# Kernel optimization log

Hardware: AMD Instinct MI355X
Metric: run time of the kernel (lower is better)

The kernel has to match this reference:

```python
import jax, jax.numpy as jnp
import numpy as np

NUM_USERS = 100_000
NUM_JOBS = 100_000
N_NODES = NUM_USERS + NUM_JOBS
E = 3_200_000
D = 64  # embedding_dim == hidden_dim
B = 16_384


def setup_inputs() -> dict:
    key = jax.random.key(0)
    ks = jax.random.split(key, 10)
    edge_index = jax.random.randint(ks[0], (2, E), 0, N_NODES, dtype=jnp.int64)
    user_indices = jax.random.randint(ks[1], (B,), 0, NUM_USERS, dtype=jnp.int64)
    job_indices = jax.random.randint(ks[2], (B,), 0, NUM_JOBS, dtype=jnp.int64)
    # parameters (match reset_parameters: embeddings std=0.1, xavier pred, zero bias)
    user_emb_w = 0.1 * jax.random.normal(ks[3], (NUM_USERS, D), dtype=jnp.float32)
    job_emb_w = 0.1 * jax.random.normal(ks[4], (NUM_JOBS, D), dtype=jnp.float32)
    W1 = jax.random.normal(ks[5], (D, D), dtype=jnp.float32) / np.sqrt(D)
    b1 = jnp.zeros((D,), dtype=jnp.float32)
    W2 = jax.random.normal(ks[6], (D, D), dtype=jnp.float32) / np.sqrt(D)
    b2 = jnp.zeros((D,), dtype=jnp.float32)
    lim = np.sqrt(6.0 / (2 * D + 1))
    pred_w = jax.random.uniform(ks[7], (2 * D, 1), dtype=jnp.float32, minval=-lim, maxval=lim)
    pred_b = jnp.zeros((1,), dtype=jnp.float32)
    return {
        "edge_index": edge_index, "user_indices": user_indices, "job_indices": job_indices,
        "user_emb_w": user_emb_w, "job_emb_w": job_emb_w,
        "W1": W1, "b1": b1, "W2": W2, "b2": b2,
        "pred_w": pred_w, "pred_b": pred_b,
    }


def reference(edge_index, user_indices, job_indices, user_emb_w, job_emb_w, W1, b1, W2, b2, pred_w, pred_b):
    num_users = user_emb_w.shape[0]
    n = num_users + job_emb_w.shape[0]
    x = jnp.concatenate([user_emb_w, job_emb_w], axis=0)  # [N, D]

    # GCNConv (PyG defaults): add self-loops, symmetric D^-1/2 (A+I) D^-1/2 normalization
    loops = jnp.arange(n, dtype=edge_index.dtype)
    row = jnp.concatenate([edge_index[0], loops])  # source nodes
    col = jnp.concatenate([edge_index[1], loops])  # target nodes
    deg = jax.ops.segment_sum(jnp.ones_like(col, dtype=x.dtype), col, num_segments=n)
    dinv = jnp.where(deg > 0, jax.lax.rsqrt(jnp.maximum(deg, 1e-12)), 0.0)
    norm = dinv[row] * dinv[col]  # [E+N]

    def gcn_conv(h, W, b):
        h = h @ W                                   # [N, D]
        msg = h[row] * norm[:, None]                # gather + scale, [E+N, D]
        agg = jax.ops.segment_sum(msg, col, num_segments=n)  # scatter-add
        return agg + b

    x = jax.nn.relu(gcn_conv(x, W1, b1))  # dropout is identity at inference
    x = gcn_conv(x, W2, b2)

    user_emb = x[user_indices]                      # [B, D]
    job_emb = x[num_users + job_indices]            # [B, D]
    combined = jnp.concatenate([user_emb, job_emb], axis=1)  # [B, 2D]
    return (combined @ pred_w + pred_b)[:, 0]       # [B]
```

## Files before the change

### kernel.cpp

```cpp
#include <hip/hip_runtime.h>
#include <hip/hip_fp16.h>

#define D 64
#define BSHIFT 10
#define BMASK ((1 << BSHIFT) - 1)
#define NBUK_MAX 256
#define T_TILE 6144
#define CAP 20480

#if defined(__has_builtin)
#if __has_builtin(__builtin_amdgcn_fdot2)
#define HAVE_FDOT2 1
#endif
#endif

typedef _Float16 h2f __attribute__((ext_vector_type(2)));
typedef _Float16 half8v __attribute__((ext_vector_type(8)));
typedef float f4v __attribute__((ext_vector_type(4)));

__device__ __forceinline__ int wave_iscan(int v, int lane) {
#pragma unroll
    for (int off = 1; off < 64; off <<= 1) {
        int u = __shfl_up(v, off, 64);
        if (lane >= off) v += u;
    }
    return v;
}

__device__ __forceinline__ int block_escan(int v, int tid, int* wtot ) {
    int lane = tid & 63, w = tid >> 6;
    int inc = wave_iscan(v, lane);
    if (lane == 63) wtot[w] = inc;
    __syncthreads();
    int addv = 0;
#pragma unroll
    for (int q = 0; q < 4; q++) addv += (q < w) ? wtot[q] : 0;
    return inc - v + addv;
}

__device__ __forceinline__ float4 h4_to_f4(uint2 u) {
    __half2 a = *(__half2*)&u.x, b = *(__half2*)&u.y;
    float2 fa = __half22float2(a), fb = __half22float2(b);
    return make_float4(fa.x, fa.y, fb.x, fb.y);
}

__device__ __forceinline__ void acc_u2(float* acc, uint2 u) {
#ifdef HAVE_FDOT2
    h2f a0, a1;
    __builtin_memcpy(&a0, &u.x, 4);
    __builtin_memcpy(&a1, &u.y, 4);
    const h2f LO = {(_Float16)1.0f, (_Float16)0.0f};
    const h2f HI = {(_Float16)0.0f, (_Float16)1.0f};
    acc[0] = __builtin_amdgcn_fdot2(a0, LO, acc[0], false);
    acc[1] = __builtin_amdgcn_fdot2(a0, HI, acc[1], false);
    acc[2] = __builtin_amdgcn_fdot2(a1, LO, acc[2], false);
    acc[3] = __builtin_amdgcn_fdot2(a1, HI, acc[3], false);
#else
    float4 v = h4_to_f4(u);
    acc[0] += v.x; acc[1] += v.y; acc[2] += v.z; acc[3] += v.w;
#endif
}

__device__ __forceinline__ void acc_u4(float* acc, uint4 u) {
    uint2 a; a.x = u.x; a.y = u.y;
    uint2 b; b.x = u.z; b.y = u.w;
    acc_u2(acc, a);
    acc_u2(acc + 4, b);
}


__global__ __launch_bounds__(256) void k_bin(const int* __restrict__ row, const int* __restrict__ col,
                                             int E, int* __restrict__ bbase,
                                             unsigned* __restrict__ ebuf, int nbuk,
                                             const float* __restrict__ W1, const float* __restrict__ W2,
                                             __half* __restrict__ WT1, __half* __restrict__ WT2) {
    __shared__ int hist4[4][NBUK_MAX];
    __shared__ int sexcl[NBUK_MAX];
    __shared__ int cur4[4][NBUK_MAX];
    __shared__ int gbase[NBUK_MAX];
    __shared__ int wtot[4];
    __shared__ unsigned stage[T_TILE];
    __shared__ unsigned char sbuk[T_TILE];
    int tid = threadIdx.x;
    int w = tid >> 6;
    int tile0 = blockIdx.x * T_TILE;
    int cnt = min(T_TILE, E - tile0);

    if (blockIdx.x < 2) {
        const float* Ws = blockIdx.x ? W2 : W1;
        __half* Wd = blockIdx.x ? WT2 : WT1;
#pragma unroll
        for (int i = 0; i < 16; i++) {
            int f = i * 256 + tid;
            int k = f >> 6, c = f & 63;
            Wd[c * 64 + k] = __float2half(Ws[f]);
        }
    }

#pragma unroll
    for (int q = 0; q < 4; q++) hist4[q][tid] = 0;
    __syncthreads();
    for (int i = tid; i < cnt; i += 256)
        atomicAdd(&hist4[w][col[tile0 + i] >> BSHIFT], 1);
    __syncthreads();

    int h0 = hist4[0][tid], h1 = hist4[1][tid], h2 = hist4[2][tid], h3 = hist4[3][tid];
    int v = h0 + h1 + h2 + h3;
    int excl = block_escan(v, tid, wtot);
    sexcl[tid] = excl;
    cur4[0][tid] = excl;
    cur4[1][tid] = excl + h0;
    cur4[2][tid] = excl + h0 + h1;
    cur4[3][tid] = excl + h0 + h1 + h2;
    gbase[tid] = (v > 0 && tid < nbuk) ? (tid * CAP + atomicAdd(&bbase[tid], v)) : 0;
    __syncthreads();

    for (int i = tid; i < cnt; i += 256) {
        int r = row[tile0 + i];
        int c = col[tile0 + i];
        int b = c >> BSHIFT;
        int p = atomicAdd(&cur4[w][b], 1);
        stage[p] = ((unsigned)(c & BMASK) << 18) | (unsigned)r;
        sbuk[p] = (unsigned char)b;
    }
    __syncthreads();

    for (int i = tid; i < cnt; i += 256) {
        int b = sbuk[i];
        int gpos = gbase[b] + (i - sexcl[b]);
        ebuf[gpos] = stage[i];
    }
}


__global__ __launch_bounds__(256) void k_csr2a(const unsigned* __restrict__ ebuf,
                                               const int* __restrict__ bbase, int N,
                                               int2* __restrict__ rps, float* __restrict__ dinv,
                                               __half* __restrict__ h, __half* __restrict__ hs2) {
    __shared__ int lcnt[1 << BSHIFT];
    __shared__ int wtot[4];
    int tid = threadIdx.x;
    int c0 = blockIdx.x << BSHIFT;
    int nn = min(1 << BSHIFT, N - c0);
    int e0 = blockIdx.x * CAP, e1 = e0 + bbase[blockIdx.x];

    if (blockIdx.x == 0 && tid < 32) {
        uint2 z; z.x = 0u; z.y = 0u;
        if (tid < 16) *(uint2*)(h + (size_t)N * D + tid * 4) = z;
        else *(uint2*)(hs2 + (size_t)N * D + (tid - 16) * 4) = z;
    }

    for (int i = tid; i < (1 << BSHIFT); i += 256) lcnt[i] = 0;
    __syncthreads();
    for (int j = e0 + tid; j < e1; j += 256)
        atomicAdd(&lcnt[ebuf[j] >> 18], 1);
    __syncthreads();

    int c[4]; int s = 0;
#pragma unroll
    for (int i = 0; i < 4; i++) { c[i] = lcnt[tid * 4 + i]; s += c[i]; }
    int run = block_escan(s, tid, wtot);
#pragma unroll
    for (int i = 0; i < 4; i++) {
        int idx = tid * 4 + i;
        if (idx < nn) {
            int st = e0 + run;
            rps[c0 + idx] = make_int2(st, st + c[i]);
            dinv[c0 + idx] = rsqrtf((float)(c[i] + 1));
        }
        run += c[i];
    }
}


__device__ __forceinline__ void stage_Wt(const __half* __restrict__ WTg, __half* __restrict__ Wt, int tid) {
#pragma unroll
    for (int i = 0; i < 2; i++) {
        int f = (i * 256 + tid) * 8;
        int c = f >> 6, k = f & 63;
        *(half8v*)(Wt + c * 72 + k) = *(const half8v*)(WTg + f);
    }
}

__device__ __forceinline__ void gemm_compute(const __half* __restrict__ Xh, const __half* __restrict__ Wt,
                                             int n0, int N, const float* __restrict__ dinv,
                                             __half* __restrict__ out, int tid) {
    int lane = tid & 63;
    int wv = tid >> 6;
    int n16 = lane & 15, quad = lane >> 4;
    const __half* Xw = Xh + (wv * 16) * 72;
    half8v a0 = *(const half8v*)(Xw + n16 * 72 + quad * 8);
    half8v a1 = *(const half8v*)(Xw + n16 * 72 + quad * 8 + 32);
    f4v acc[4];
#pragma unroll
    for (int ct = 0; ct < 4; ct++) {
        acc[ct] = (f4v){0.f, 0.f, 0.f, 0.f};
        const __half* wp = Wt + (ct * 16 + n16) * 72;
        half8v b0 = *(const half8v*)(wp + quad * 8);
        half8v b1 = *(const half8v*)(wp + quad * 8 + 32);
        acc[ct] = __builtin_amdgcn_mfma_f32_16x16x32_f16(a0, b0, acc[ct], 0, 0, 0);
        acc[ct] = __builtin_amdgcn_mfma_f32_16x16x32_f16(a1, b1, acc[ct], 0, 0, 0);
    }
#pragma unroll
    for (int r = 0; r < 4; r++) {
        int node = n0 + wv * 16 + quad * 4 + r;
        if (node < N) {
            float dv = dinv[node];
#pragma unroll
            for (int ct = 0; ct < 4; ct++)
                out[(size_t)node * D + ct * 16 + n16] = __float2half(acc[ct][r] * dv);
        }
    }
}


__global__ __launch_bounds__(256) void k_csr2b_gemm1(const unsigned* __restrict__ ebuf,
                                                     const int2* __restrict__ rps,
                                                     const int* __restrict__ bbase,
                                                     int N, int nbuk, int* __restrict__ srcs,
                                                     const float* __restrict__ xu, const float* __restrict__ xj,
                                                     int U, const __half* __restrict__ WT1,
                                                     const float* __restrict__ dinv, __half* __restrict__ h) {
    __shared__ __align__(16) __half Xh[64 * 72];
    __shared__ __align__(16) __half Wt[64 * 72];
    int tid = threadIdx.x;
    if ((int)blockIdx.x < nbuk) {
        int* lcur = (int*)Xh;
        int c0 = blockIdx.x << BSHIFT;
        int e0 = blockIdx.x * CAP, e1 = e0 + bbase[blockIdx.x];
        for (int i = tid; i < (1 << BSHIFT); i += 256)
            lcur[i] = (c0 + i < N) ? rps[c0 + i].x : 0;
        __syncthreads();
        for (int j = e0 + tid; j < e1; j += 256) {
            unsigned pk = ebuf[j];
            int p = atomicAdd(&lcur[pk >> 18], 1);
            srcs[p] = (int)(pk & 0x3ffffu);
        }
    } else {
        int n0 = ((int)blockIdx.x - nbuk) * 64;
        stage_Wt(WT1, Wt, tid);
#pragma unroll
        for (int i = 0; i < 4; i++) {
            int e4 = i * 256 + tid;
            int nl = e4 >> 4, k4 = e4 & 15;
            int nn = n0 + nl;
            uint2 st; st.x = 0u; st.y = 0u;
            if (nn < N) {
                const float* src = (nn < U) ? (xu + (size_t)nn * D) : (xj + (size_t)(nn - U) * D);
                float4 v = *(const float4*)(src + k4 * 4);
                __half2 p0 = __floats2half2_rn(v.x, v.y);
                __half2 p1 = __floats2half2_rn(v.z, v.w);
                st.x = *(unsigned*)&p0; st.y = *(unsigned*)&p1;
            }
            *(uint2*)(Xh + nl * 72 + k4 * 4) = st;
        }
        __syncthreads();
        gemm_compute(Xh, Wt, n0, N, dinv, h, tid);
    }
}


__device__ __forceinline__ void gather8(float* acc, const __half* __restrict__ hs,
                                        const int2* __restrict__ rps,
                                        const int* __restrict__ srcs,
                                        int node, int N, int g, int t) {
    const __half* hp = hs + t * 8;
    int2 r = rps[node];
    int e0 = r.x, deg = r.y - r.x;
    for (int cb = 0; cb < deg; cb += 8) {
        int sv = (cb + t < deg) ? srcs[e0 + cb + t] : N;
        int base = g * 8;
        int s0 = __shfl(sv, base + 0, 64);
        int s1 = __shfl(sv, base + 1, 64);
        int s2 = __shfl(sv, base + 2, 64);
        int s3 = __shfl(sv, base + 3, 64);
        int s4 = __shfl(sv, base + 4, 64);
        int s5 = __shfl(sv, base + 5, 64);
        int s6 = __shfl(sv, base + 6, 64);
        int s7 = __shfl(sv, base + 7, 64);
        uint4 u0 = *(const uint4*)(hp + (size_t)s0 * D);
        uint4 u1 = *(const uint4*)(hp + (size_t)s1 * D);
        uint4 u2 = *(const uint4*)(hp + (size_t)s2 * D);
        uint4 u3 = *(const uint4*)(hp + (size_t)s3 * D);
        uint4 u4 = *(const uint4*)(hp + (size_t)s4 * D);
        uint4 u5 = *(const uint4*)(hp + (size_t)s5 * D);
        uint4 u6 = *(const uint4*)(hp + (size_t)s6 * D);
        uint4 u7 = *(const uint4*)(hp + (size_t)s7 * D);
        acc_u4(acc, u0);
        acc_u4(acc, u1);
        acc_u4(acc, u2);
        acc_u4(acc, u3);
        acc_u4(acc, u4);
        acc_u4(acc, u5);
        acc_u4(acc, u6);
        acc_u4(acc, u7);
    }
}


__global__ __launch_bounds__(256) void k_agg_gemm2(const __half* __restrict__ hs, const float* __restrict__ dinv,
                                                   const int2* __restrict__ rps, const int* __restrict__ srcs,
                                                   const float* __restrict__ bias, const __half* __restrict__ WT2,
                                                   int N, __half* __restrict__ hs2) {
    __shared__ __align__(16) __half Xh[64 * 72];
    __shared__ __align__(16) __half Wt[64 * 72];
    int tid = threadIdx.x;
    int lane = tid & 63;
    int w = tid >> 6;
    int g = lane >> 3, t = lane & 7;
    int n0 = blockIdx.x * 64;

    stage_Wt(WT2, Wt, tid);

    float4 ba = *(const float4*)(bias + t * 8);
    float4 bb = *(const float4*)(bias + t * 8 + 4);
#pragma unroll
    for (int rr = 0; rr < 2; rr++) {
        int nl = w * 16 + rr * 8 + g;
        int node = n0 + nl;
        uint4 st; st.x = 0u; st.y = 0u; st.z = 0u; st.w = 0u;
        if (node < N) {
            float acc[8] = {0.f, 0.f, 0.f, 0.f, 0.f, 0.f, 0.f, 0.f};
            gather8(acc, hs, rps, srcs, node, N, g, t);
            uint4 su = *(const uint4*)(hs + (size_t)node * D + t * 8);
            float4 sa = h4_to_f4(make_uint2(su.x, su.y));
            float4 sb = h4_to_f4(make_uint2(su.z, su.w));
            float dv = dinv[node];
            float o0 = fmaxf((acc[0] + sa.x) * dv + ba.x, 0.f);
            float o1 = fmaxf((acc[1] + sa.y) * dv + ba.y, 0.f);
            float o2 = fmaxf((acc[2] + sa.z) * dv + ba.z, 0.f);
            float o3 = fmaxf((acc[3] + sa.w) * dv + ba.w, 0.f);
            float o4 = fmaxf((acc[4] + sb.x) * dv + bb.x, 0.f);
            float o5 = fmaxf((acc[5] + sb.y) * dv + bb.y, 0.f);
            float o6 = fmaxf((acc[6] + sb.z) * dv + bb.z, 0.f);
            float o7 = fmaxf((acc[7] + sb.w) * dv + bb.w, 0.f);
            __half2 p0 = __floats2half2_rn(o0, o1);
            __half2 p1 = __floats2half2_rn(o2, o3);
            __half2 p2 = __floats2half2_rn(o4, o5);
            __half2 p3 = __floats2half2_rn(o6, o7);
            st.x = *(unsigned*)&p0; st.y = *(unsigned*)&p1;
            st.z = *(unsigned*)&p2; st.w = *(unsigned*)&p3;
        }
        *(uint4*)(Xh + nl * 72 + t * 8) = st;
    }
    __syncthreads();
    gemm_compute(Xh, Wt, n0, N, dinv, hs2, tid);
}


__global__ __launch_bounds__(256) void k_pred(const __half* __restrict__ hs2, const float* __restrict__ dinv,
                                              const int2* __restrict__ rps, const int* __restrict__ srcs,
                                              const float* __restrict__ b2, const float* __restrict__ pw,
                                              const float* __restrict__ pb,
                                              const int* __restrict__ uidx, const int* __restrict__ jidx,
                                              int U, int N, int B, float* __restrict__ out) {
    int tid = threadIdx.x;
    int lane = tid & 63;
    int g = lane >> 3, t = lane & 7;
    int pair = blockIdx.x * 16 + (tid >> 6) * 4 + (g >> 1);
    if (pair >= B) return;
    int side = g & 1;
    int c = side ? (U + jidx[pair]) : uidx[pair];
    float acc[8] = {0.f, 0.f, 0.f, 0.f, 0.f, 0.f, 0.f, 0.f};
    gather8(acc, hs2, rps, srcs, c, N, g, t);
    uint4 su = *(const uint4*)(hs2 + (size_t)c * D + t * 8);
    float4 sa = h4_to_f4(make_uint2(su.x, su.y));
    float4 sb = h4_to_f4(make_uint2(su.z, su.w));
    float4 bva = *(const float4*)(b2 + t * 8);
    float4 bvb = *(const float4*)(b2 + t * 8 + 4);
    float dv = dinv[c];
    float4 wa = *(const float4*)(pw + side * 64 + t * 8);
    float4 wb = *(const float4*)(pw + side * 64 + t * 8 + 4);
    float vx = ((acc[0] + sa.x) * dv + bva.x) * wa.x
             + ((acc[1] + sa.y) * dv + bva.y) * wa.y
             + ((acc[2] + sa.z) * dv + bva.z) * wa.z
             + ((acc[3] + sa.w) * dv + bva.w) * wa.w
             + ((acc[4] + sb.x) * dv + bvb.x) * wb.x
             + ((acc[5] + sb.y) * dv + bvb.y) * wb.y
             + ((acc[6] + sb.z) * dv + bvb.z) * wb.z
             + ((acc[7] + sb.w) * dv + bvb.w) * wb.w;
    vx += __shfl_xor(vx, 1, 64); vx += __shfl_xor(vx, 2, 64);
    vx += __shfl_xor(vx, 4, 64);
    vx += __shfl_xor(vx, 8, 64);
    if ((lane & 15) == 0) out[pair] = vx + pb[0];
}


extern "C" void kernel_launch(void* const* d_in, const int* in_sizes, int n_in,
                              void* d_out, int out_size, void* d_ws, size_t ws_size,
                              hipStream_t stream) {
    const int*   edge = (const int*)d_in[0];
    const int*   uidx = (const int*)d_in[1];
    const int*   jidx = (const int*)d_in[2];
    const float* xu   = (const float*)d_in[3];
    const float* xj   = (const float*)d_in[4];
    const float* W1   = (const float*)d_in[5];
    const float* b1   = (const float*)d_in[6];
    const float* W2   = (const float*)d_in[7];
    const float* b2   = (const float*)d_in[8];
    const float* pw   = (const float*)d_in[9];
    const float* pb   = (const float*)d_in[10];
    float* out = (float*)d_out;

    int E = in_sizes[0] / 2;
    int B = in_sizes[1];
    int U = in_sizes[3] / D;
    int J = in_sizes[4] / D;
    int N = U + J;
    int nbuk = (N + (1 << BSHIFT) - 1) >> BSHIFT;
    const int* row = edge;
    const int* col = edge + E;

    char* p = (char*)d_ws;
    auto alloc = [&](size_t bytes) -> void* {
        void* q = (void*)p;
        p += (bytes + 255) / 256 * 256;
        return q;
    };
    size_t capsz = (size_t)nbuk * CAP * 4;
    size_t hs2sz = (size_t)(N + 1) * D * 2;
    int*    bbase   = (int*)alloc(256 * 4);
    int2*   rps     = (int2*)alloc((size_t)N * 8);
    float*  dinv    = (float*)alloc((size_t)N * 4);
    int*    srcs    = (int*)alloc(capsz);
    __half* h       = (__half*)alloc((size_t)(N + 1) * D * 2);
    __half* hs2     = (__half*)alloc(hs2sz > capsz ? hs2sz : capsz);
    __half* WT1     = (__half*)alloc((size_t)D * D * 2);
    __half* WT2     = (__half*)alloc((size_t)D * D * 2);
    unsigned* ebuf  = (unsigned*)hs2;

    hipMemsetAsync(bbase, 0, 256 * 4, stream);

    k_bin<<<(E + T_TILE - 1) / T_TILE, 256, 0, stream>>>(row, col, E, bbase, ebuf, nbuk,
                                                         W1, W2, WT1, WT2);
    k_csr2a<<<nbuk, 256, 0, stream>>>(ebuf, bbase, N, rps, dinv, h, hs2);

    k_csr2b_gemm1<<<nbuk + (N + 63) / 64, 256, 0, stream>>>(ebuf, rps, bbase, N, nbuk, srcs,
                                                            xu, xj, U, WT1, dinv, h);

    k_agg_gemm2<<<(N + 63) / 64, 256, 0, stream>>>(h, dinv, rps, srcs, b1, WT2, N, hs2);

    k_pred<<<(B + 15) / 16, 256, 0, stream>>>(hs2, dinv, rps, srcs, b2, pw, pb, uidx, jidx, U, N, B, out);
}
```

Baseline: 280.7 us.

## Fuse CSR count and fill into gemm1 kernel, fold dinv into layer-1 gather

Merges the CSR counting/scan kernel into the CSR fill + GEMM1 kernel. GEMM1 then no longer depends on dinv, so its output is left unscaled and the source-side dinv is applied per edge during the layer-1 gather. This removes one launch and lets the GEMM blocks run alongside CSR construction. k_bin now holds each thread's edges in registers, so row/col are read from global memory once instead of twice. The cost is an extra dinv gather and FMA per edge in layer 1, plus higher register pressure in k_bin.

```diff
diff --git a/kernel.cpp b/kernel.cpp
--- a/kernel.cpp
+++ b/kernel.cpp
@@ -6,6 +6,7 @@
 #define BMASK ((1 << BSHIFT) - 1)
 #define NBUK_MAX 256
 #define T_TILE 6144
+#define EPT 24
 #define CAP 20480
 
 #if defined(__has_builtin)
@@ -66,6 +67,19 @@
     uint2 b; b.x = u.z; b.y = u.w;
     acc_u2(acc, a);
     acc_u2(acc + 4, b);
+}
+
+__device__ __forceinline__ void acc_u4f(float* acc, uint4 u, float s) {
+    float4 a = h4_to_f4(make_uint2(u.x, u.y));
+    float4 b = h4_to_f4(make_uint2(u.z, u.w));
+    acc[0] = fmaf(a.x, s, acc[0]);
+    acc[1] = fmaf(a.y, s, acc[1]);
+    acc[2] = fmaf(a.z, s, acc[2]);
+    acc[3] = fmaf(a.w, s, acc[3]);
+    acc[4] = fmaf(b.x, s, acc[4]);
+    acc[5] = fmaf(b.y, s, acc[5]);
+    acc[6] = fmaf(b.z, s, acc[6]);
+    acc[7] = fmaf(b.w, s, acc[7]);
 }
 
 
@@ -97,11 +111,25 @@
         }
     }
 
+    unsigned pk[EPT];
+    int bk[EPT];
+
 #pragma unroll
     for (int q = 0; q < 4; q++) hist4[q][tid] = 0;
     __syncthreads();
-    for (int i = tid; i < cnt; i += 256)
-        atomicAdd(&hist4[w][col[tile0 + i] >> BSHIFT], 1);
+#pragma unroll
+    for (int j = 0; j < EPT; j++) {
+        int i = tid + j * 256;
+        if (i < cnt) {
+            int r = row[tile0 + i];
+            int c = col[tile0 + i];
+            bk[j] = c >> BSHIFT;
+            pk[j] = ((unsigned)(c & BMASK) << 18) | (unsigned)r;
+            atomicAdd(&hist4[w][bk[j]], 1);
+        } else {
+            bk[j] = -1;
+        }
+    }
     __syncthreads();
 
     int h0 = hist4[0][tid], h1 = hist4[1][tid], h2 = hist4[2][tid], h3 = hist4[3][tid];
@@ -115,13 +143,13 @@
     gbase[tid] = (v > 0 && tid < nbuk) ? (tid * CAP + atomicAdd(&bbase[tid], v)) : 0;
     __syncthreads();
 
-    for (int i = tid; i < cnt; i += 256) {
-        int r = row[tile0 + i];
-        int c = col[tile0 + i];
-        int b = c >> BSHIFT;
-        int p = atomicAdd(&cur4[w][b], 1);
-        stage[p] = ((unsigned)(c & BMASK) << 18) | (unsigned)r;
-        sbuk[p] = (unsigned char)b;
+#pragma unroll
+    for (int j = 0; j < EPT; j++) {
+        if (bk[j] >= 0) {
+            int p = atomicAdd(&cur4[w][bk[j]], 1);
+            stage[p] = pk[j];
+            sbuk[p] = (unsigned char)bk[j];
+        }
     }
     __syncthreads();
 
@@ -133,46 +161,6 @@
 }
 
 
-__global__ __launch_bounds__(256) void k_csr2a(const unsigned* __restrict__ ebuf,
-                                               const int* __restrict__ bbase, int N,
-                                               int2* __restrict__ rps, float* __restrict__ dinv,
-                                               __half* __restrict__ h, __half* __restrict__ hs2) {
-    __shared__ int lcnt[1 << BSHIFT];
-    __shared__ int wtot[4];
-    int tid = threadIdx.x;
-    int c0 = blockIdx.x << BSHIFT;
-    int nn = min(1 << BSHIFT, N - c0);
-    int e0 = blockIdx.x * CAP, e1 = e0 + bbase[blockIdx.x];
-
-    if (blockIdx.x == 0 && tid < 32) {
-        uint2 z; z.x = 0u; z.y = 0u;
-        if (tid < 16) *(uint2*)(h + (size_t)N * D + tid * 4) = z;
-        else *(uint2*)(hs2 + (size_t)N * D + (tid - 16) * 4) = z;
-    }
-
-    for (int i = tid; i < (1 << BSHIFT); i += 256) lcnt[i] = 0;
-    __syncthreads();
-    for (int j = e0 + tid; j < e1; j += 256)
-        atomicAdd(&lcnt[ebuf[j] >> 18], 1);
-    __syncthreads();
-
-    int c[4]; int s = 0;
-#pragma unroll
-    for (int i = 0; i < 4; i++) { c[i] = lcnt[tid * 4 + i]; s += c[i]; }
-    int run = block_escan(s, tid, wtot);
-#pragma unroll
-    for (int i = 0; i < 4; i++) {
-        int idx = tid * 4 + i;
-        if (idx < nn) {
-            int st = e0 + run;
-            rps[c0 + idx] = make_int2(st, st + c[i]);
-            dinv[c0 + idx] = rsqrtf((float)(c[i] + 1));
-        }
-        run += c[i];
-    }
-}
-
-
 __device__ __forceinline__ void stage_Wt(const __half* __restrict__ WTg, __half* __restrict__ Wt, int tid) {
 #pragma unroll
     for (int i = 0; i < 2; i++) {
@@ -183,7 +171,7 @@
 }
 
 __device__ __forceinline__ void gemm_compute(const __half* __restrict__ Xh, const __half* __restrict__ Wt,
-                                             int n0, int N, const float* __restrict__ dinv,
+                                             int n0, int N, const float* __restrict__ dinvp,
                                              __half* __restrict__ out, int tid) {
     int lane = tid & 63;
     int wv = tid >> 6;
@@ -205,7 +193,7 @@
     for (int r = 0; r < 4; r++) {
         int node = n0 + wv * 16 + quad * 4 + r;
         if (node < N) {
-            float dv = dinv[node];
+            float dv = dinvp ? dinvp[node] : 1.0f;
 #pragma unroll
             for (int ct = 0; ct < 4; ct++)
                 out[(size_t)node * D + ct * 16 + n16] = __float2half(acc[ct][r] * dv);
@@ -214,26 +202,56 @@
 }
 
 
-__global__ __launch_bounds__(256) void k_csr2b_gemm1(const unsigned* __restrict__ ebuf,
-                                                     const int2* __restrict__ rps,
-                                                     const int* __restrict__ bbase,
-                                                     int N, int nbuk, int* __restrict__ srcs,
-                                                     const float* __restrict__ xu, const float* __restrict__ xj,
-                                                     int U, const __half* __restrict__ WT1,
-                                                     const float* __restrict__ dinv, __half* __restrict__ h) {
+__global__ __launch_bounds__(256) void k_csr_gemm1(const unsigned* __restrict__ ebuf,
+                                                   const int* __restrict__ bbase,
+                                                   int N, int nbuk,
+                                                   int2* __restrict__ rps, float* __restrict__ dinv,
+                                                   int* __restrict__ srcs,
+                                                   const float* __restrict__ xu, const float* __restrict__ xj,
+                                                   int U, const __half* __restrict__ WT1,
+                                                   __half* __restrict__ h, __half* __restrict__ hs2) {
     __shared__ __align__(16) __half Xh[64 * 72];
     __shared__ __align__(16) __half Wt[64 * 72];
+    __shared__ int wtot[4];
     int tid = threadIdx.x;
     if ((int)blockIdx.x < nbuk) {
-        int* lcur = (int*)Xh;
+        int* lcnt = (int*)Xh;
         int c0 = blockIdx.x << BSHIFT;
+        int nn = min(1 << BSHIFT, N - c0);
         int e0 = blockIdx.x * CAP, e1 = e0 + bbase[blockIdx.x];
-        for (int i = tid; i < (1 << BSHIFT); i += 256)
-            lcur[i] = (c0 + i < N) ? rps[c0 + i].x : 0;
+
+        if (blockIdx.x == 0) {
+            uint2 z; z.x = 0u; z.y = 0u;
+            if (tid < 16) *(uint2*)(h + (size_t)N * D + tid * 4) = z;
+            else if (tid < 32) *(uint2*)(hs2 + (size_t)N * D + (tid - 16) * 4) = z;
+            else if (tid == 32) dinv[N] = 0.0f;
+        }
+
+        for (int i = tid; i < (1 << BSHIFT); i += 256) lcnt[i] = 0;
+        __syncthreads();
+        for (int j = e0 + tid; j < e1; j += 256)
+            atomicAdd(&lcnt[ebuf[j] >> 18], 1);
+        __syncthreads();
+
+        int c[4]; int s = 0;
+#pragma unroll
+        for (int i = 0; i < 4; i++) { c[i] = lcnt[tid * 4 + i]; s += c[i]; }
+        int run = block_escan(s, tid, wtot);
+#pragma unroll
+        for (int i = 0; i < 4; i++) {
+            int idx = tid * 4 + i;
+            int st = e0 + run;
+            if (idx < nn) {
+                rps[c0 + idx] = make_int2(st, st + c[i]);
+                dinv[c0 + idx] = rsqrtf((float)(c[i] + 1));
+            }
+            lcnt[idx] = st;
+            run += c[i];
+        }
         __syncthreads();
         for (int j = e0 + tid; j < e1; j += 256) {
             unsigned pk = ebuf[j];
-            int p = atomicAdd(&lcur[pk >> 18], 1);
+            int p = atomicAdd(&lcnt[pk >> 18], 1);
             srcs[p] = (int)(pk & 0x3ffffu);
         }
     } else {
@@ -255,12 +273,14 @@
             *(uint2*)(Xh + nl * 72 + k4 * 4) = st;
         }
         __syncthreads();
-        gemm_compute(Xh, Wt, n0, N, dinv, h, tid);
-    }
-}
-
-
+        gemm_compute(Xh, Wt, n0, N, nullptr, h, tid);
+    }
+}
+
+
+template <bool FOLD>
 __device__ __forceinline__ void gather8(float* acc, const __half* __restrict__ hs,
+                                        const float* __restrict__ dinv,
                                         const int2* __restrict__ rps,
                                         const int* __restrict__ srcs,
                                         int node, int N, int g, int t) {
@@ -269,6 +289,8 @@
     int e0 = r.x, deg = r.y - r.x;
     for (int cb = 0; cb < deg; cb += 8) {
         int sv = (cb + t < deg) ? srcs[e0 + cb + t] : N;
+        float fv = 0.0f;
+        if (FOLD) fv = dinv[sv];
         int base = g * 8;
         int s0 = __shfl(sv, base + 0, 64);
         int s1 = __shfl(sv, base + 1, 64);
@@ -286,14 +308,33 @@
         uint4 u5 = *(const uint4*)(hp + (size_t)s5 * D);
         uint4 u6 = *(const uint4*)(hp + (size_t)s6 * D);
         uint4 u7 = *(const uint4*)(hp + (size_t)s7 * D);
-        acc_u4(acc, u0);
-        acc_u4(acc, u1);
-        acc_u4(acc, u2);
-        acc_u4(acc, u3);
-        acc_u4(acc, u4);
-        acc_u4(acc, u5);
-        acc_u4(acc, u6);
-        acc_u4(acc, u7);
+        if (FOLD) {
+            float d0 = __shfl(fv, base + 0, 64);
+            float d1 = __shfl(fv, base + 1, 64);
+            float d2 = __shfl(fv, base + 2, 64);
+            float d3 = __shfl(fv, base + 3, 64);
+            float d4 = __shfl(fv, base + 4, 64);
+            float d5 = __shfl(fv, base + 5, 64);
+            float d6 = __shfl(fv, base + 6, 64);
+            float d7 = __shfl(fv, base + 7, 64);
+            acc_u4f(acc, u0, d0);
+            acc_u4f(acc, u1, d1);
+            acc_u4f(acc, u2, d2);
+            acc_u4f(acc, u3, d3);
+            acc_u4f(acc, u4, d4);
+            acc_u4f(acc, u5, d5);
+            acc_u4f(acc, u6, d6);
+            acc_u4f(acc, u7, d7);
+        } else {
+            acc_u4(acc, u0);
+            acc_u4(acc, u1);
+            acc_u4(acc, u2);
+            acc_u4(acc, u3);
+            acc_u4(acc, u4);
+            acc_u4(acc, u5);
+            acc_u4(acc, u6);
+            acc_u4(acc, u7);
+        }
     }
 }
 
@@ -321,19 +362,19 @@
         uint4 st; st.x = 0u; st.y = 0u; st.z = 0u; st.w = 0u;
         if (node < N) {
             float acc[8] = {0.f, 0.f, 0.f, 0.f, 0.f, 0.f, 0.f, 0.f};
-            gather8(acc, hs, rps, srcs, node, N, g, t);
+            gather8<true>(acc, hs, dinv, rps, srcs, node, N, g, t);
             uint4 su = *(const uint4*)(hs + (size_t)node * D + t * 8);
             float4 sa = h4_to_f4(make_uint2(su.x, su.y));
             float4 sb = h4_to_f4(make_uint2(su.z, su.w));
             float dv = dinv[node];
-            float o0 = fmaxf((acc[0] + sa.x) * dv + ba.x, 0.f);
-            float o1 = fmaxf((acc[1] + sa.y) * dv + ba.y, 0.f);
-            float o2 = fmaxf((acc[2] + sa.z) * dv + ba.z, 0.f);
-            float o3 = fmaxf((acc[3] + sa.w) * dv + ba.w, 0.f);
-            float o4 = fmaxf((acc[4] + sb.x) * dv + bb.x, 0.f);
-            float o5 = fmaxf((acc[5] + sb.y) * dv + bb.y, 0.f);
-            float o6 = fmaxf((acc[6] + sb.z) * dv + bb.z, 0.f);
-            float o7 = fmaxf((acc[7] + sb.w) * dv + bb.w, 0.f);
+            float o0 = fmaxf((acc[0] + sa.x * dv) * dv + ba.x, 0.f);
+            float o1 = fmaxf((acc[1] + sa.y * dv) * dv + ba.y, 0.f);
+            float o2 = fmaxf((acc[2] + sa.z * dv) * dv + ba.z, 0.f);
+            float o3 = fmaxf((acc[3] + sa.w * dv) * dv + ba.w, 0.f);
+            float o4 = fmaxf((acc[4] + sb.x * dv) * dv + bb.x, 0.f);
+            float o5 = fmaxf((acc[5] + sb.y * dv) * dv + bb.y, 0.f);
+            float o6 = fmaxf((acc[6] + sb.z * dv) * dv + bb.z, 0.f);
+            float o7 = fmaxf((acc[7] + sb.w * dv) * dv + bb.w, 0.f);
             __half2 p0 = __floats2half2_rn(o0, o1);
             __half2 p1 = __floats2half2_rn(o2, o3);
             __half2 p2 = __floats2half2_rn(o4, o5);
@@ -362,7 +403,7 @@
     int side = g & 1;
     int c = side ? (U + jidx[pair]) : uidx[pair];
     float acc[8] = {0.f, 0.f, 0.f, 0.f, 0.f, 0.f, 0.f, 0.f};
-    gather8(acc, hs2, rps, srcs, c, N, g, t);
+    gather8<false>(acc, hs2, dinv, rps, srcs, c, N, g, t);
     uint4 su = *(const uint4*)(hs2 + (size_t)c * D + t * 8);
     float4 sa = h4_to_f4(make_uint2(su.x, su.y));
     float4 sb = h4_to_f4(make_uint2(su.z, su.w));
@@ -421,7 +462,7 @@
     size_t hs2sz = (size_t)(N + 1) * D * 2;
     int*    bbase   = (int*)alloc(256 * 4);
     int2*   rps     = (int2*)alloc((size_t)N * 8);
-    float*  dinv    = (float*)alloc((size_t)N * 4);
+    float*  dinv    = (float*)alloc((size_t)(N + 1) * 4);
     int*    srcs    = (int*)alloc(capsz);
     __half* h       = (__half*)alloc((size_t)(N + 1) * D * 2);
     __half* hs2     = (__half*)alloc(hs2sz > capsz ? hs2sz : capsz);
@@ -433,10 +474,9 @@
 
     k_bin<<<(E + T_TILE - 1) / T_TILE, 256, 0, stream>>>(row, col, E, bbase, ebuf, nbuk,
                                                          W1, W2, WT1, WT2);
-    k_csr2a<<<nbuk, 256, 0, stream>>>(ebuf, bbase, N, rps, dinv, h, hs2);
-
-    k_csr2b_gemm1<<<nbuk + (N + 63) / 64, 256, 0, stream>>>(ebuf, rps, bbase, N, nbuk, srcs,
-                                                            xu, xj, U, WT1, dinv, h);
+
+    k_csr_gemm1<<<nbuk + (N + 63) / 64, 256, 0, stream>>>(ebuf, bbase, N, nbuk, rps, dinv, srcs,
+                                                          xu, xj, U, WT1, h, hs2);
 
     k_agg_gemm2<<<(N + 63) / 64, 256, 0, stream>>>(h, dinv, rps, srcs, b1, WT2, N, hs2);
 
```

New measurement: 271.6 us. 1.03x faster.

## Fold CSR row-pointer pass into gemm1 kernel and count degrees via global atomics

Applied to the files above, without the earlier changes.

Removes the separate k_csr2a launch by merging its per-bucket counting and scan into the CSR scatter blocks of the gemm1 kernel. The GEMM1 blocks now take their degree scaling from a global degree array, filled with per-edge atomics in k_bin, instead of waiting on dinv. k_bin also keeps row/col packed in registers between passes so edges are read once, and its tile is halved so more blocks launch. The cost is 3.2M extra global atomics and a larger memset in exchange for one fewer launch and dependency.

```diff
diff --git a/kernel.cpp b/kernel.cpp
--- a/kernel.cpp
+++ b/kernel.cpp
@@ -5,7 +5,8 @@
 #define BSHIFT 10
 #define BMASK ((1 << BSHIFT) - 1)
 #define NBUK_MAX 256
-#define T_TILE 6144
+#define T_TILE 3072
+#define EPT 12
 #define CAP 20480
 
 #if defined(__has_builtin)
@@ -70,7 +71,7 @@
 
 
 __global__ __launch_bounds__(256) void k_bin(const int* __restrict__ row, const int* __restrict__ col,
-                                             int E, int* __restrict__ bbase,
+                                             int E, int* __restrict__ bbase, int* __restrict__ deg,
                                              unsigned* __restrict__ ebuf, int nbuk,
                                              const float* __restrict__ W1, const float* __restrict__ W2,
                                              __half* __restrict__ WT1, __half* __restrict__ WT2) {
@@ -97,11 +98,26 @@
         }
     }
 
+    unsigned pk[EPT];
+    int bk[EPT];
+
 #pragma unroll
     for (int q = 0; q < 4; q++) hist4[q][tid] = 0;
     __syncthreads();
-    for (int i = tid; i < cnt; i += 256)
-        atomicAdd(&hist4[w][col[tile0 + i] >> BSHIFT], 1);
+#pragma unroll
+    for (int j = 0; j < EPT; j++) {
+        int i = tid + j * 256;
+        if (i < cnt) {
+            int r = row[tile0 + i];
+            int c = col[tile0 + i];
+            bk[j] = c >> BSHIFT;
+            pk[j] = ((unsigned)(c & BMASK) << 18) | (unsigned)r;
+            atomicAdd(&hist4[w][bk[j]], 1);
+            atomicAdd(&deg[c], 1);
+        } else {
+            bk[j] = -1;
+        }
+    }
     __syncthreads();
 
     int h0 = hist4[0][tid], h1 = hist4[1][tid], h2 = hist4[2][tid], h3 = hist4[3][tid];
@@ -115,13 +131,13 @@
     gbase[tid] = (v > 0 && tid < nbuk) ? (tid * CAP + atomicAdd(&bbase[tid], v)) : 0;
     __syncthreads();
 
-    for (int i = tid; i < cnt; i += 256) {
-        int r = row[tile0 + i];
-        int c = col[tile0 + i];
-        int b = c >> BSHIFT;
-        int p = atomicAdd(&cur4[w][b], 1);
-        stage[p] = ((unsigned)(c & BMASK) << 18) | (unsigned)r;
-        sbuk[p] = (unsigned char)b;
+#pragma unroll
+    for (int j = 0; j < EPT; j++) {
+        if (bk[j] >= 0) {
+            int p = atomicAdd(&cur4[w][bk[j]], 1);
+            stage[p] = pk[j];
+            sbuk[p] = (unsigned char)bk[j];
+        }
     }
     __syncthreads();
 
@@ -133,46 +149,6 @@
 }
 
 
-__global__ __launch_bounds__(256) void k_csr2a(const unsigned* __restrict__ ebuf,
-                                               const int* __restrict__ bbase, int N,
-                                               int2* __restrict__ rps, float* __restrict__ dinv,
-                                               __half* __restrict__ h, __half* __restrict__ hs2) {
-    __shared__ int lcnt[1 << BSHIFT];
-    __shared__ int wtot[4];
-    int tid = threadIdx.x;
-    int c0 = blockIdx.x << BSHIFT;
-    int nn = min(1 << BSHIFT, N - c0);
-    int e0 = blockIdx.x * CAP, e1 = e0 + bbase[blockIdx.x];
-
-    if (blockIdx.x == 0 && tid < 32) {
-        uint2 z; z.x = 0u; z.y = 0u;
-        if (tid < 16) *(uint2*)(h + (size_t)N * D + tid * 4) = z;
-        else *(uint2*)(hs2 + (size_t)N * D + (tid - 16) * 4) = z;
-    }
-
-    for (int i = tid; i < (1 << BSHIFT); i += 256) lcnt[i] = 0;
-    __syncthreads();
-    for (int j = e0 + tid; j < e1; j += 256)
-        atomicAdd(&lcnt[ebuf[j] >> 18], 1);
-    __syncthreads();
-
-    int c[4]; int s = 0;
-#pragma unroll
-    for (int i = 0; i < 4; i++) { c[i] = lcnt[tid * 4 + i]; s += c[i]; }
-    int run = block_escan(s, tid, wtot);
-#pragma unroll
-    for (int i = 0; i < 4; i++) {
-        int idx = tid * 4 + i;
-        if (idx < nn) {
-            int st = e0 + run;
-            rps[c0 + idx] = make_int2(st, st + c[i]);
-            dinv[c0 + idx] = rsqrtf((float)(c[i] + 1));
-        }
-        run += c[i];
-    }
-}
-
-
 __device__ __forceinline__ void stage_Wt(const __half* __restrict__ WTg, __half* __restrict__ Wt, int tid) {
 #pragma unroll
     for (int i = 0; i < 2; i++) {
@@ -183,7 +159,8 @@
 }
 
 __device__ __forceinline__ void gemm_compute(const __half* __restrict__ Xh, const __half* __restrict__ Wt,
-                                             int n0, int N, const float* __restrict__ dinv,
+                                             int n0, int N, const int* __restrict__ degp,
+                                             const float* __restrict__ dinvp,
                                              __half* __restrict__ out, int tid) {
     int lane = tid & 63;
     int wv = tid >> 6;
@@ -205,7 +182,9 @@
     for (int r = 0; r < 4; r++) {
         int node = n0 + wv * 16 + quad * 4 + r;
         if (node < N) {
-            float dv = dinv[node];
+            float dv = 1.0f;
+            if (degp) dv = rsqrtf((float)(degp[node] + 1));
+            else if (dinvp) dv = dinvp[node];
 #pragma unroll
             for (int ct = 0; ct < 4; ct++)
                 out[(size_t)node * D + ct * 16 + n16] = __float2half(acc[ct][r] * dv);
@@ -214,26 +193,56 @@
 }
 
 
-__global__ __launch_bounds__(256) void k_csr2b_gemm1(const unsigned* __restrict__ ebuf,
-                                                     const int2* __restrict__ rps,
-                                                     const int* __restrict__ bbase,
-                                                     int N, int nbuk, int* __restrict__ srcs,
-                                                     const float* __restrict__ xu, const float* __restrict__ xj,
-                                                     int U, const __half* __restrict__ WT1,
-                                                     const float* __restrict__ dinv, __half* __restrict__ h) {
+__global__ __launch_bounds__(256) void k_csr_gemm1(const unsigned* __restrict__ ebuf,
+                                                   const int* __restrict__ bbase,
+                                                   const int* __restrict__ deg,
+                                                   int N, int nbuk,
+                                                   int2* __restrict__ rps, float* __restrict__ dinv,
+                                                   int* __restrict__ srcs,
+                                                   const float* __restrict__ xu, const float* __restrict__ xj,
+                                                   int U, const __half* __restrict__ WT1,
+                                                   __half* __restrict__ h, __half* __restrict__ hs2) {
     __shared__ __align__(16) __half Xh[64 * 72];
     __shared__ __align__(16) __half Wt[64 * 72];
+    __shared__ int wtot[4];
     int tid = threadIdx.x;
     if ((int)blockIdx.x < nbuk) {
-        int* lcur = (int*)Xh;
+        int* lcnt = (int*)Xh;
         int c0 = blockIdx.x << BSHIFT;
+        int nn = min(1 << BSHIFT, N - c0);
         int e0 = blockIdx.x * CAP, e1 = e0 + bbase[blockIdx.x];
-        for (int i = tid; i < (1 << BSHIFT); i += 256)
-            lcur[i] = (c0 + i < N) ? rps[c0 + i].x : 0;
+
+        if (blockIdx.x == 0) {
+            uint2 z; z.x = 0u; z.y = 0u;
+            if (tid < 16) *(uint2*)(h + (size_t)N * D + tid * 4) = z;
+            else if (tid < 32) *(uint2*)(hs2 + (size_t)N * D + (tid - 16) * 4) = z;
+        }
+
+        for (int i = tid; i < (1 << BSHIFT); i += 256) lcnt[i] = 0;
+        __syncthreads();
+        for (int j = e0 + tid; j < e1; j += 256)
+            atomicAdd(&lcnt[ebuf[j] >> 18], 1);
+        __syncthreads();
+
+        int c[4]; int s = 0;
+#pragma unroll
+        for (int i = 0; i < 4; i++) { c[i] = lcnt[tid * 4 + i]; s += c[i]; }
+        int run = block_escan(s, tid, wtot);
+#pragma unroll
+        for (int i = 0; i < 4; i++) {
+            int idx = tid * 4 + i;
+            int st = e0 + run;
+            if (idx < nn) {
+                rps[c0 + idx] = make_int2(st, st + c[i]);
+                dinv[c0 + idx] = rsqrtf((float)(c[i] + 1));
+            }
+            lcnt[idx] = st;
+            run += c[i];
+        }
         __syncthreads();
         for (int j = e0 + tid; j < e1; j += 256) {
             unsigned pk = ebuf[j];
-            int p = atomicAdd(&lcur[pk >> 18], 1);
+            int p = atomicAdd(&lcnt[pk >> 18], 1);
             srcs[p] = (int)(pk & 0x3ffffu);
         }
     } else {
@@ -255,7 +264,7 @@
             *(uint2*)(Xh + nl * 72 + k4 * 4) = st;
         }
         __syncthreads();
-        gemm_compute(Xh, Wt, n0, N, dinv, h, tid);
+        gemm_compute(Xh, Wt, n0, N, deg, nullptr, h, tid);
     }
 }
 
@@ -344,7 +353,7 @@
         *(uint4*)(Xh + nl * 72 + t * 8) = st;
     }
     __syncthreads();
-    gemm_compute(Xh, Wt, n0, N, dinv, hs2, tid);
+    gemm_compute(Xh, Wt, n0, N, nullptr, dinv, hs2, tid);
 }
 
 
@@ -420,6 +429,7 @@
     size_t capsz = (size_t)nbuk * CAP * 4;
     size_t hs2sz = (size_t)(N + 1) * D * 2;
     int*    bbase   = (int*)alloc(256 * 4);
+    int*    deg     = (int*)alloc((size_t)N * 4);
     int2*   rps     = (int2*)alloc((size_t)N * 8);
     float*  dinv    = (float*)alloc((size_t)N * 4);
     int*    srcs    = (int*)alloc(capsz);
@@ -429,14 +439,13 @@
     __half* WT2     = (__half*)alloc((size_t)D * D * 2);
     unsigned* ebuf  = (unsigned*)hs2;
 
-    hipMemsetAsync(bbase, 0, 256 * 4, stream);
-
-    k_bin<<<(E + T_TILE - 1) / T_TILE, 256, 0, stream>>>(row, col, E, bbase, ebuf, nbuk,
+    hipMemsetAsync(bbase, 0, (size_t)((char*)(deg + N) - (char*)bbase), stream);
+
+    k_bin<<<(E + T_TILE - 1) / T_TILE, 256, 0, stream>>>(row, col, E, bbase, deg, ebuf, nbuk,
                                                          W1, W2, WT1, WT2);
-    k_csr2a<<<nbuk, 256, 0, stream>>>(ebuf, bbase, N, rps, dinv, h, hs2);
-
-    k_csr2b_gemm1<<<nbuk + (N + 63) / 64, 256, 0, stream>>>(ebuf, rps, bbase, N, nbuk, srcs,
-                                                            xu, xj, U, WT1, dinv, h);
+
+    k_csr_gemm1<<<nbuk + (N + 63) / 64, 256, 0, stream>>>(ebuf, bbase, deg, N, nbuk, rps, dinv, srcs,
+                                                          xu, xj, U, WT1, h, hs2);
 
     k_agg_gemm2<<<(N + 63) / 64, 256, 0, stream>>>(h, dinv, rps, srcs, b1, WT2, N, hs2);
 
```

New measurement: 376.7 us. 1.34x slower.

## Fold prediction weights into layer-2 GEMM and cache edge data in registers

Applied to the files above, without the earlier changes.

The second GCN layer output is only used through a dot product with the prediction weights, and that product is linear. So the GEMM2 epilogue now projects each node onto the user and job halves of pred_w, giving two scalars per node instead of a 64-wide fp16 row. k_pred then gathers scalars over neighbors rather than 128-byte rows, which cuts gather traffic in the final aggregation. Separately, the binning kernel keeps each thread's edges in registers (24 per thread), so the second pass does not reload row and col from global memory; this raises register pressure.

```diff
diff --git a/kernel.cpp b/kernel.cpp
--- a/kernel.cpp
+++ b/kernel.cpp
@@ -6,6 +6,7 @@
 #define BMASK ((1 << BSHIFT) - 1)
 #define NBUK_MAX 256
 #define T_TILE 6144
+#define EPT 24
 #define CAP 20480
 
 #if defined(__has_builtin)
@@ -97,11 +98,25 @@
         }
     }
 
+    unsigned pk[EPT];
+    int bk[EPT];
+
 #pragma unroll
     for (int q = 0; q < 4; q++) hist4[q][tid] = 0;
     __syncthreads();
-    for (int i = tid; i < cnt; i += 256)
-        atomicAdd(&hist4[w][col[tile0 + i] >> BSHIFT], 1);
+#pragma unroll
+    for (int j = 0; j < EPT; j++) {
+        int i = tid + j * 256;
+        if (i < cnt) {
+            int r = row[tile0 + i];
+            int c = col[tile0 + i];
+            bk[j] = c >> BSHIFT;
+            pk[j] = ((unsigned)(c & BMASK) << 18) | (unsigned)r;
+            atomicAdd(&hist4[w][bk[j]], 1);
+        } else {
+            bk[j] = -1;
+        }
+    }
     __syncthreads();
 
     int h0 = hist4[0][tid], h1 = hist4[1][tid], h2 = hist4[2][tid], h3 = hist4[3][tid];
@@ -115,13 +130,13 @@
     gbase[tid] = (v > 0 && tid < nbuk) ? (tid * CAP + atomicAdd(&bbase[tid], v)) : 0;
     __syncthreads();
 
-    for (int i = tid; i < cnt; i += 256) {
-        int r = row[tile0 + i];
-        int c = col[tile0 + i];
-        int b = c >> BSHIFT;
-        int p = atomicAdd(&cur4[w][b], 1);
-        stage[p] = ((unsigned)(c & BMASK) << 18) | (unsigned)r;
-        sbuk[p] = (unsigned char)b;
+#pragma unroll
+    for (int j = 0; j < EPT; j++) {
+        if (bk[j] >= 0) {
+            int p = atomicAdd(&cur4[w][bk[j]], 1);
+            stage[p] = pk[j];
+            sbuk[p] = (unsigned char)bk[j];
+        }
     }
     __syncthreads();
 
@@ -136,7 +151,7 @@
 __global__ __launch_bounds__(256) void k_csr2a(const unsigned* __restrict__ ebuf,
                                                const int* __restrict__ bbase, int N,
                                                int2* __restrict__ rps, float* __restrict__ dinv,
-                                               __half* __restrict__ h, __half* __restrict__ hs2) {
+                                               __half* __restrict__ h) {
     __shared__ int lcnt[1 << BSHIFT];
     __shared__ int wtot[4];
     int tid = threadIdx.x;
@@ -144,10 +159,9 @@
     int nn = min(1 << BSHIFT, N - c0);
     int e0 = blockIdx.x * CAP, e1 = e0 + bbase[blockIdx.x];
 
-    if (blockIdx.x == 0 && tid < 32) {
+    if (blockIdx.x == 0 && tid < 16) {
         uint2 z; z.x = 0u; z.y = 0u;
-        if (tid < 16) *(uint2*)(h + (size_t)N * D + tid * 4) = z;
-        else *(uint2*)(hs2 + (size_t)N * D + (tid - 16) * 4) = z;
+        *(uint2*)(h + (size_t)N * D + tid * 4) = z;
     }
 
     for (int i = tid; i < (1 << BSHIFT); i += 256) lcnt[i] = 0;
@@ -183,7 +197,7 @@
 }
 
 __device__ __forceinline__ void gemm_compute(const __half* __restrict__ Xh, const __half* __restrict__ Wt,
-                                             int n0, int N, const float* __restrict__ dinv,
+                                             int n0, int N, const float* __restrict__ dinvp,
                                              __half* __restrict__ out, int tid) {
     int lane = tid & 63;
     int wv = tid >> 6;
@@ -205,7 +219,7 @@
     for (int r = 0; r < 4; r++) {
         int node = n0 + wv * 16 + quad * 4 + r;
         if (node < N) {
-            float dv = dinv[node];
+            float dv = dinvp[node];
 #pragma unroll
             for (int ct = 0; ct < 4; ct++)
                 out[(size_t)node * D + ct * 16 + n16] = __float2half(acc[ct][r] * dv);
@@ -301,7 +315,8 @@
 __global__ __launch_bounds__(256) void k_agg_gemm2(const __half* __restrict__ hs, const float* __restrict__ dinv,
                                                    const int2* __restrict__ rps, const int* __restrict__ srcs,
                                                    const float* __restrict__ bias, const __half* __restrict__ WT2,
-                                                   int N, __half* __restrict__ hs2) {
+                                                   const float* __restrict__ pw, int N,
+                                                   float* __restrict__ zu, float* __restrict__ zj) {
     __shared__ __align__(16) __half Xh[64 * 72];
     __shared__ __align__(16) __half Wt[64 * 72];
     int tid = threadIdx.x;
@@ -344,11 +359,47 @@
         *(uint4*)(Xh + nl * 72 + t * 8) = st;
     }
     __syncthreads();
-    gemm_compute(Xh, Wt, n0, N, dinv, hs2, tid);
-}
-
-
-__global__ __launch_bounds__(256) void k_pred(const __half* __restrict__ hs2, const float* __restrict__ dinv,
+
+    int wv = w;
+    int n16 = lane & 15, quad = lane >> 4;
+    const __half* Xw = Xh + (wv * 16) * 72;
+    half8v a0 = *(const half8v*)(Xw + n16 * 72 + quad * 8);
+    half8v a1 = *(const half8v*)(Xw + n16 * 72 + quad * 8 + 32);
+    f4v acc[4];
+    float pwu_r[4], pwj_r[4];
+#pragma unroll
+    for (int ct = 0; ct < 4; ct++) {
+        pwu_r[ct] = pw[ct * 16 + n16];
+        pwj_r[ct] = pw[64 + ct * 16 + n16];
+        acc[ct] = (f4v){0.f, 0.f, 0.f, 0.f};
+        const __half* wp = Wt + (ct * 16 + n16) * 72;
+        half8v b0 = *(const half8v*)(wp + quad * 8);
+        half8v b1 = *(const half8v*)(wp + quad * 8 + 32);
+        acc[ct] = __builtin_amdgcn_mfma_f32_16x16x32_f16(a0, b0, acc[ct], 0, 0, 0);
+        acc[ct] = __builtin_amdgcn_mfma_f32_16x16x32_f16(a1, b1, acc[ct], 0, 0, 0);
+    }
+#pragma unroll
+    for (int r = 0; r < 4; r++) {
+        int node = n0 + wv * 16 + quad * 4 + r;
+        float dv = (node < N) ? dinv[node] : 0.0f;
+        float su = acc[0][r] * pwu_r[0] + acc[1][r] * pwu_r[1]
+                 + acc[2][r] * pwu_r[2] + acc[3][r] * pwu_r[3];
+        float sj = acc[0][r] * pwj_r[0] + acc[1][r] * pwj_r[1]
+                 + acc[2][r] * pwj_r[2] + acc[3][r] * pwj_r[3];
+        su += __shfl_xor(su, 1, 64); sj += __shfl_xor(sj, 1, 64);
+        su += __shfl_xor(su, 2, 64); sj += __shfl_xor(sj, 2, 64);
+        su += __shfl_xor(su, 4, 64); sj += __shfl_xor(sj, 4, 64);
+        su += __shfl_xor(su, 8, 64); sj += __shfl_xor(sj, 8, 64);
+        if (n16 == 0 && node < N) {
+            zu[node] = su * dv;
+            zj[node] = sj * dv;
+        }
+    }
+}
+
+
+__global__ __launch_bounds__(256) void k_pred(const float* __restrict__ zu, const float* __restrict__ zj,
+                                              const float* __restrict__ dinv,
                                               const int2* __restrict__ rps, const int* __restrict__ srcs,
                                               const float* __restrict__ b2, const float* __restrict__ pw,
                                               const float* __restrict__ pb,
@@ -361,28 +412,28 @@
     if (pair >= B) return;
     int side = g & 1;
     int c = side ? (U + jidx[pair]) : uidx[pair];
-    float acc[8] = {0.f, 0.f, 0.f, 0.f, 0.f, 0.f, 0.f, 0.f};
-    gather8(acc, hs2, rps, srcs, c, N, g, t);
-    uint4 su = *(const uint4*)(hs2 + (size_t)c * D + t * 8);
-    float4 sa = h4_to_f4(make_uint2(su.x, su.y));
-    float4 sb = h4_to_f4(make_uint2(su.z, su.w));
-    float4 bva = *(const float4*)(b2 + t * 8);
-    float4 bvb = *(const float4*)(b2 + t * 8 + 4);
-    float dv = dinv[c];
+    const float* zt = side ? zj : zu;
+
+    float4 b2a = *(const float4*)(b2 + t * 8);
+    float4 b2b = *(const float4*)(b2 + t * 8 + 4);
     float4 wa = *(const float4*)(pw + side * 64 + t * 8);
     float4 wb = *(const float4*)(pw + side * 64 + t * 8 + 4);
-    float vx = ((acc[0] + sa.x) * dv + bva.x) * wa.x
-             + ((acc[1] + sa.y) * dv + bva.y) * wa.y
-             + ((acc[2] + sa.z) * dv + bva.z) * wa.z
-             + ((acc[3] + sa.w) * dv + bva.w) * wa.w
-             + ((acc[4] + sb.x) * dv + bvb.x) * wb.x
-             + ((acc[5] + sb.y) * dv + bvb.y) * wb.y
-             + ((acc[6] + sb.z) * dv + bvb.z) * wb.z
-             + ((acc[7] + sb.w) * dv + bvb.w) * wb.w;
-    vx += __shfl_xor(vx, 1, 64); vx += __shfl_xor(vx, 2, 64);
-    vx += __shfl_xor(vx, 4, 64);
-    vx += __shfl_xor(vx, 8, 64);
-    if ((lane & 15) == 0) out[pair] = vx + pb[0];
+    float cpart = b2a.x * wa.x + b2a.y * wa.y + b2a.z * wa.z + b2a.w * wa.w
+                + b2b.x * wb.x + b2b.y * wb.y + b2b.z * wb.z + b2b.w * wb.w;
+
+    int2 r = rps[c];
+    int deg = r.y - r.x;
+    float s = 0.f;
+    for (int cb = 0; cb < deg; cb += 8) {
+        if (cb + t < deg) s += zt[srcs[r.x + cb + t]];
+    }
+    s += __shfl_xor(s, 1, 64); cpart += __shfl_xor(cpart, 1, 64);
+    s += __shfl_xor(s, 2, 64); cpart += __shfl_xor(cpart, 2, 64);
+    s += __shfl_xor(s, 4, 64); cpart += __shfl_xor(cpart, 4, 64);
+
+    float val = (s + zt[c]) * dinv[c] + cpart;
+    val += __shfl_xor(val, 8, 64);
+    if ((lane & 15) == 0) out[pair] = val + pb[0];
 }
 
 
@@ -418,27 +469,29 @@
         return q;
     };
     size_t capsz = (size_t)nbuk * CAP * 4;
-    size_t hs2sz = (size_t)(N + 1) * D * 2;
-    int*    bbase   = (int*)alloc(256 * 4);
-    int2*   rps     = (int2*)alloc((size_t)N * 8);
-    float*  dinv    = (float*)alloc((size_t)N * 4);
-    int*    srcs    = (int*)alloc(capsz);
-    __half* h       = (__half*)alloc((size_t)(N + 1) * D * 2);
-    __half* hs2     = (__half*)alloc(hs2sz > capsz ? hs2sz : capsz);
-    __half* WT1     = (__half*)alloc((size_t)D * D * 2);
-    __half* WT2     = (__half*)alloc((size_t)D * D * 2);
-    unsigned* ebuf  = (unsigned*)hs2;
+    int*      bbase = (int*)alloc(256 * 4);
+    int2*     rps   = (int2*)alloc((size_t)N * 8);
+    float*    dinv  = (float*)alloc((size_t)N * 4);
+    int*      srcs  = (int*)alloc(capsz);
+    __half*   h     = (__half*)alloc((size_t)(N + 1) * D * 2);
+    unsigned* ebuf  = (unsigned*)alloc(capsz);
+    float*    zu    = (float*)alloc((size_t)N * 4);
+    float*    zj    = (float*)alloc((size_t)N * 4);
+    __half*   WT1   = (__half*)alloc((size_t)D * D * 2);
+    __half*   WT2   = (__half*)alloc((size_t)D * D * 2);
 
     hipMemsetAsync(bbase, 0, 256 * 4, stream);
 
     k_bin<<<(E + T_TILE - 1) / T_TILE, 256, 0, stream>>>(row, col, E, bbase, ebuf, nbuk,
                                                          W1, W2, WT1, WT2);
-    k_csr2a<<<nbuk, 256, 0, stream>>>(ebuf, bbase, N, rps, dinv, h, hs2);
+
+    k_csr2a<<<nbuk, 256, 0, stream>>>(ebuf, bbase, N, rps, dinv, h);
 
     k_csr2b_gemm1<<<nbuk + (N + 63) / 64, 256, 0, stream>>>(ebuf, rps, bbase, N, nbuk, srcs,
                                                             xu, xj, U, WT1, dinv, h);
 
-    k_agg_gemm2<<<(N + 63) / 64, 256, 0, stream>>>(h, dinv, rps, srcs, b1, WT2, N, hs2);
-
-    k_pred<<<(B + 15) / 16, 256, 0, stream>>>(hs2, dinv, rps, srcs, b2, pw, pb, uidx, jidx, U, N, B, out);
-}
+    k_agg_gemm2<<<(N + 63) / 64, 256, 0, stream>>>(h, dinv, rps, srcs, b1, WT2, pw, N, zu, zj);
+
+    k_pred<<<(B + 15) / 16, 256, 0, stream>>>(zu, zj, dinv, rps, srcs, b2, pw, pb,
+                                              uidx, jidx, U, N, B, out);
+}
```

After: 259.0 us. 7.7% less time.
